# Optimization experiments

Measured on AMD Instinct MI355X. Metric: run time of the kernel, lower is better.

Reference implementation:

```python
import jax, jax.numpy as jnp
import numpy as np

NEG = -9.0e15

def gat_layer(X, adj_mask, W, Wb, a1, a2, ab):
    # X: [N, Fin]; W: [Fin, Fout]; a1,a2: [Fout]; ab: scalar
    h = X @ W + Wb                                   # [N, Fout]
    # a([h_i || h_j]) = h_i@a1 + h_j@a2 + ab  (decomposition of concat+linear)
    e = jax.nn.leaky_relu((h @ a1)[:, None] + (h @ a2)[None, :] + ab,
                          negative_slope=0.2)        # [N, N]
    e = jnp.where(adj_mask, e, NEG)
    attn = jax.nn.softmax(e, axis=1)                 # [N, N]
    return jax.nn.elu(attn @ h)                      # [N, Fout]

def setup_inputs() -> dict:
    key = jax.random.key(0)
    ks = jax.random.split(key, 12)
    N, Fin, Fh, H, Fout = 4096, 512, 128, 4, 64
    X = jax.random.normal(ks[0], (N, Fin), dtype=jnp.float32)
    adjacency_matrix = jax.random.randint(ks[1], (N, N), 0, 2, dtype=jnp.int32)
    s_in = 1.0 / np.sqrt(Fin)
    s_a = 1.0 / np.sqrt(2 * Fh)
    W_h  = jax.random.uniform(ks[2], (H, Fin, Fh), jnp.float32, -s_in, s_in)
    b_h  = jax.random.uniform(ks[3], (H, Fh), jnp.float32, -s_in, s_in)
    a1_h = jax.random.uniform(ks[4], (H, Fh), jnp.float32, -s_a, s_a)
    a2_h = jax.random.uniform(ks[5], (H, Fh), jnp.float32, -s_a, s_a)
    ab_h = jax.random.uniform(ks[6], (H,), jnp.float32, -s_a, s_a)
    Fcat = H * Fh
    s_c = 1.0 / np.sqrt(Fcat)
    s_ao = 1.0 / np.sqrt(2 * Fout)
    W_o  = jax.random.uniform(ks[7], (Fcat, Fout), jnp.float32, -s_c, s_c)
    b_o  = jax.random.uniform(ks[8], (Fout,), jnp.float32, -s_c, s_c)
    a1_o = jax.random.uniform(ks[9], (Fout,), jnp.float32, -s_ao, s_ao)
    a2_o = jax.random.uniform(ks[10], (Fout,), jnp.float32, -s_ao, s_ao)
    ab_o = jax.random.uniform(ks[11], (), jnp.float32, -s_ao, s_ao)
    return {"X": X, "adjacency_matrix": adjacency_matrix,
            "W_h": W_h, "b_h": b_h, "a1_h": a1_h, "a2_h": a2_h, "ab_h": ab_h,
            "W_o": W_o, "b_o": b_o, "a1_o": a1_o, "a2_o": a2_o, "ab_o": ab_o}

def reference(X, adjacency_matrix, W_h, b_h, a1_h, a2_h, ab_h,
              W_o, b_o, a1_o, a2_o, ab_o):
    adj_mask = adjacency_matrix > 0
    # per-head attention layers, vmapped over heads
    heads = jax.vmap(gat_layer, in_axes=(None, None, 0, 0, 0, 0, 0))(
        X, adj_mask, W_h, b_h, a1_h, a2_h, ab_h)      # [H, N, Fh]
    H, N, Fh = heads.shape
    x = jnp.transpose(heads, (1, 0, 2)).reshape(N, H * Fh)  # concat along features
    x = gat_layer(x, adj_mask, W_o, b_o, a1_o, a2_o, ab_o)  # [N, Fout]
    return jax.nn.log_softmax(x, axis=1)
```

## Files before the change

### kernel.cpp

```cpp
#include <hip/hip_runtime.h>
#include <math.h>

#define NN 4096

using f32x4  = __attribute__((ext_vector_type(4))) float;
using bf16x4 = __attribute__((ext_vector_type(4))) __bf16;
using bf16x8 = __attribute__((ext_vector_type(8))) __bf16;

__device__ __forceinline__ void barrier_lgkm() {
    asm volatile("s_waitcnt lgkmcnt(0)\ns_barrier" ::: "memory");
}

template<int FH>
__device__ __forceinline__ void stage_tile(const __bf16* __restrict__ hgp,
                                           __bf16* dst, int tid) {
#pragma unroll
    for (int it = 0; it < FH / 32; it++) {
        int c = tid + it * 256;
        int f = c >> 3, sl = c & 7;
        int g = sl ^ (f & 7);
        __builtin_amdgcn_global_load_lds(
            (const __attribute__((address_space(1))) void*)(hgp + (size_t)f * NN + g * 8),
            (__attribute__((address_space(3))) void*)(dst + (size_t)c * 8), 16, 0, 0);
    }
}

__device__ __forceinline__ void stage_g(const __bf16* __restrict__ base, int ldk,
                                        __bf16* dst, int tid) {
#pragma unroll
    for (int it = 0; it < 2; it++) {
        int c = tid + it * 256;
        int f = c >> 3, sl = c & 7;
        int g = sl ^ (f & 7);
        __builtin_amdgcn_global_load_lds(
            (const __attribute__((address_space(1))) void*)(base + (size_t)f * ldk + g * 8),
            (__attribute__((address_space(3))) void*)(dst + (size_t)c * 8), 16, 0, 0);
    }
}

__global__ void pack_adj_kernel(const int* __restrict__ adj,
                                unsigned long long* __restrict__ bits) {
    int gw = (blockIdx.x * blockDim.x + threadIdx.x) >> 6;
    int lane = threadIdx.x & 63;
    int v = adj[(size_t)gw * 64 + lane];
    unsigned long long m = __ballot(v > 0);
    if (lane == 0) bits[gw] = m;
}

__global__ void prepack_kernel(const float* __restrict__ W_h, const float* __restrict__ b_h,
                               const float* __restrict__ W_o,
                               __bf16* __restrict__ Bt1, float* __restrict__ biasp,
                               __bf16* __restrict__ Bt2) {
    int idx = blockIdx.x * 256 + threadIdx.x;
    {
        int n = idx >> 9, k = idx & 511;
        int h = n >> 7, f = n & 127;
        Bt1[idx] = (__bf16)W_h[(size_t)h * 512 * 128 + k * 128 + f];
    }
    if (idx < 64 * 512) {
        int n = idx >> 9, k = idx & 511;
        Bt2[idx] = (__bf16)W_o[k * 64 + n];
    }
    if (idx < 512) biasp[idx] = b_h[idx];
}

__global__ void cast_bf16_kernel(const float* __restrict__ src, __bf16* __restrict__ dst) {
    int i = blockIdx.x * 256 + threadIdx.x;
    f32x4 v = *(const f32x4*)(src + (size_t)i * 4);
    bf16x4 o;
#pragma unroll
    for (int q = 0; q < 4; q++) o[q] = (__bf16)v[q];
    *(bf16x4*)(dst + (size_t)i * 4) = o;
}

__global__ __launch_bounds__(256) void gemm_fused_kernel(
    const __bf16* __restrict__ A, const __bf16* __restrict__ Bt,
    const float* __restrict__ bias,
    const float* __restrict__ a1, const float* __restrict__ a2,
    __bf16* __restrict__ Ht, float* __restrict__ s1, float* __restrict__ s2,
    int M, int N, int K)
{
    __shared__ __attribute__((aligned(16))) __bf16 As[2][64 * 64];
    __shared__ __attribute__((aligned(16))) __bf16 Bs[2][64 * 64];
    const int tid = threadIdx.x, w = tid >> 6, l = tid & 63, o = l >> 4, rl = l & 15;
    const int bm = blockIdx.y * 64, bn = blockIdx.x * 64;
    f32x4 acc[4] = {};
    stage_g(A + (size_t)bm * K, K, &As[0][0], tid);
    stage_g(Bt + (size_t)bn * K, K, &Bs[0][0], tid);
    const int KB = K / 64;
    for (int kb = 0; kb < KB; kb++) {
        int b = kb & 1;
        __syncthreads();
        if (kb + 1 < KB) {
            stage_g(A + (size_t)bm * K + (kb + 1) * 64, K, &As[b ^ 1][0], tid);
            stage_g(Bt + (size_t)bn * K + (kb + 1) * 64, K, &Bs[b ^ 1][0], tid);
        }
#pragma unroll
        for (int kt = 0; kt < 2; kt++) {
            int ra = w * 16 + rl;
            int cg = kt * 4 + o;
            bf16x8 af = *(const bf16x8*)(&As[b][(ra * 8 + (cg ^ (ra & 7))) * 8]);
#pragma unroll
            for (int nt = 0; nt < 4; nt++) {
                int rb = nt * 16 + rl;
                bf16x8 bfr = *(const bf16x8*)(&Bs[b][(rb * 8 + (cg ^ (rb & 7))) * 8]);
                acc[nt] = __builtin_amdgcn_mfma_f32_16x16x32_bf16(af, bfr, acc[nt], 0, 0, 0);
            }
        }
    }
    const int head = bn >> 7;
    const int row_base = bm + w * 16 + o * 4;
    float p1[4] = {0.f, 0.f, 0.f, 0.f}, p2[4] = {0.f, 0.f, 0.f, 0.f};
#pragma unroll
    for (int nt = 0; nt < 4; nt++) {
        int col = bn + nt * 16 + rl;
        float bv = bias[col];
        float a1v = a1[col], a2v = a2[col];
        bf16x4 hv;
#pragma unroll
        for (int r4 = 0; r4 < 4; r4++) {
            float h = acc[nt][r4] + bv;
            hv[r4] = (__bf16)h;
            p1[r4] += h * a1v;
            p2[r4] += h * a2v;
        }
        *(bf16x4*)(Ht + (size_t)col * M + row_base) = hv;
    }
#pragma unroll
    for (int r4 = 0; r4 < 4; r4++)
#pragma unroll
        for (int off = 1; off < 16; off <<= 1) {
            p1[r4] += __shfl_xor(p1[r4], off, 64);
            p2[r4] += __shfl_xor(p2[r4], off, 64);
        }
    if (rl == 0)
#pragma unroll
        for (int r4 = 0; r4 < 4; r4++) {
            atomicAdd(&s1[(size_t)head * M + row_base + r4], p1[r4]);
            atomicAdd(&s2[(size_t)head * M + row_base + r4], p2[r4]);
        }
}

__global__ void smax_kernel(const float* __restrict__ s2, float* __restrict__ s2max) {
    const float* p = s2 + (size_t)blockIdx.x * NN;
    int t = threadIdx.x;
    float m = -INFINITY;
    for (int i = t; i < NN; i += 256) m = fmaxf(m, p[i]);
#pragma unroll
    for (int off = 1; off < 64; off <<= 1) m = fmaxf(m, __shfl_xor(m, off, 64));
    __shared__ float red[4];
    if ((t & 63) == 0) red[t >> 6] = m;
    __syncthreads();
    if (t == 0) s2max[blockIdx.x] = fmaxf(fmaxf(red[0], red[1]), fmaxf(red[2], red[3]));
}

template<int FH, int JSPLIT>
__global__ __launch_bounds__(256, 4) void attn_kernel(
    const __bf16* __restrict__ Htg,
    const unsigned long long* __restrict__ adj_bits,
    const float* __restrict__ s1_all, const float* __restrict__ s2_all,
    const float* __restrict__ s2max_all, const float* __restrict__ ab_all,
    __bf16* __restrict__ accp,
    float* __restrict__ lg,
    int ldo)
{
    constexpr int NJT = NN / 64 / JSPLIT;
    constexpr int NTW = FH / 64;
    const int head = blockIdx.y;
    const int js   = blockIdx.z;
    const int row0 = blockIdx.x * 64;
    const int jt0  = js * NJT;
    const int tid = threadIdx.x;
    const int w = tid >> 6, l = tid & 63, o = l >> 4, rl = l & 15;
    const int myrow = row0 + w * 16 + rl;

    __shared__ __attribute__((aligned(16))) __bf16 hbuf[2][FH * 64];
    __shared__ __attribute__((aligned(16))) __bf16 plds[8 * 64 * 8];

    const float* s2 = s2_all + (size_t)head * NN;
    const __bf16* hg = Htg + (size_t)head * FH * NN;
    const float s1r = s1_all[(size_t)head * NN + myrow] + ab_all[head];
    float mrow; { float x = s1r + s2max_all[head]; mrow = fmaxf(x, 0.2f * x); }
    float lacc = 0.f;
    f32x4 acc[4][NTW] = {};

    stage_tile<FH>(hg + (size_t)jt0 * 64, &hbuf[0][0], tid);

    for (int jl = 0; jl < NJT; jl++) {
        const int b = jl & 1;
        const int jt = jt0 + jl;
        unsigned long long aw = adj_bits[(size_t)myrow * 64 + jt];
        bf16x8 freg[2];
#pragma unroll
        for (int kt = 0; kt < 2; kt++) {
            unsigned int mbyte = (unsigned int)(aw >> ((kt * 4 + o) * 8)) & 0xFFu;
            int jb = jt * 64 + kt * 32 + o * 8;
            f32x4 sa = *(const f32x4*)(s2 + jb);
            f32x4 sb = *(const f32x4*)(s2 + jb + 4);
            float ps = 0.f;
#pragma unroll
            for (int q = 0; q < 8; q++) {
                float s2q = (q < 4) ? sa[q] : sb[q - 4];
                float x = s1r + s2q;
                float e = fmaxf(x, 0.2f * x);
                float p = ((mbyte >> q) & 1u) ? __expf(e - mrow) : 0.f;
                freg[kt][q] = (__bf16)p;
                ps += p;
            }
            ps += __shfl_xor(ps, 16, 64);
            ps += __shfl_xor(ps, 32, 64);
            lacc += ps;
            *(bf16x8*)(&plds[((w * 2 + kt) * 64 + l) * 8]) = freg[kt];
        }
        __syncthreads();
        if (jl + 1 < NJT)
            stage_tile<FH>(hg + (size_t)(jt + 1) * 64, &hbuf[b ^ 1][0], tid);
        bf16x8 bfr[2][NTW];
#pragma unroll
        for (int kt = 0; kt < 2; kt++)
#pragma unroll
            for (int ntl = 0; ntl < NTW; ntl++) {
                int f = (w * NTW + ntl) * 16 + rl;
                int slot = (kt * 4 + o) ^ (rl & 7);
                bfr[kt][ntl] = *(const bf16x8*)(&hbuf[b][(f * 8 + slot) * 8]);
            }
#pragma unroll
        for (int mt = 0; mt < 4; mt++)
#pragma unroll
            for (int kt = 0; kt < 2; kt++) {
                bf16x8 af = (mt == w) ? freg[kt]
                          : *(const bf16x8*)(&plds[((mt * 2 + kt) * 64 + l) * 8]);
#pragma unroll
                for (int ntl = 0; ntl < NTW; ntl++)
                    acc[mt][ntl] = __builtin_amdgcn_mfma_f32_16x16x32_bf16(
                        af, bfr[kt][ntl], acc[mt][ntl], 0, 0, 0);
            }
        barrier_lgkm();
    }
    if (l < 16) lg[((size_t)head * JSPLIT + js) * NN + row0 + w * 16 + l] = lacc;
#pragma unroll
    for (int mt = 0; mt < 4; mt++)
#pragma unroll
        for (int ntl = 0; ntl < NTW; ntl++)
#pragma unroll
            for (int r4 = 0; r4 < 4; r4++) {
                int grow = row0 + mt * 16 + o * 4 + r4;
                int gcol = head * FH + (w * NTW + ntl) * 16 + rl;
                accp[((size_t)js * NN + grow) * ldo + gcol] = (__bf16)acc[mt][ntl][r4];
            }
}

__global__ void combine1_kernel(const __bf16* __restrict__ accp, const float* __restrict__ lg,
                                __bf16* __restrict__ outb) {
    int gid = blockIdx.x * 256 + threadIdx.x;
    int row = gid >> 7, c4 = (gid & 127) * 4;
    int head = c4 >> 7;
    float lsum = 0.f;
#pragma unroll
    for (int js = 0; js < 4; js++) lsum += lg[((size_t)head * 4 + js) * NN + row];
    float inv = lsum > 0.f ? 1.f / lsum : 0.f;
    float v[4] = {0.f, 0.f, 0.f, 0.f};
#pragma unroll
    for (int js = 0; js < 4; js++) {
        bf16x4 t = *(const bf16x4*)(accp + ((size_t)js * NN + row) * 512 + c4);
#pragma unroll
        for (int q = 0; q < 4; q++) v[q] += (float)t[q];
    }
    bf16x4 ob;
#pragma unroll
    for (int q = 0; q < 4; q++) {
        float x = v[q] * inv;
        x = x > 0.f ? x : __expf(x) - 1.f;
        ob[q] = (__bf16)x;
    }
    *(bf16x4*)(outb + (size_t)row * 512 + c4) = ob;
}

__global__ void combine2_kernel(const __bf16* __restrict__ accp, const float* __restrict__ lg,
                                float* __restrict__ out) {
    int row = (blockIdx.x * 256 + threadIdx.x) >> 6;
    int lane = threadIdx.x & 63;
    if (row >= NN) return;
    float lsum = 0.f, v = 0.f;
#pragma unroll
    for (int js = 0; js < 16; js++) {
        lsum += lg[(size_t)js * NN + row];
        v += (float)accp[((size_t)js * NN + row) * 64 + lane];
    }
    float inv = lsum > 0.f ? 1.f / lsum : 0.f;
    v *= inv;
    v = v > 0.f ? v : __expf(v) - 1.f;
    float m = v;
#pragma unroll
    for (int off = 1; off < 64; off <<= 1) m = fmaxf(m, __shfl_xor(m, off, 64));
    float ex = __expf(v - m);
    float s = ex;
#pragma unroll
    for (int off = 1; off < 64; off <<= 1) s += __shfl_xor(s, off, 64);
    out[(size_t)row * 64 + lane] = v - m - __logf(s);
}

extern "C" void kernel_launch(void* const* d_in, const int* in_sizes, int n_in,
                              void* d_out, int out_size, void* d_ws, size_t ws_size,
                              hipStream_t stream) {
    const float* X    = (const float*)d_in[0];
    const int*   adj  = (const int*)d_in[1];
    const float* W_h  = (const float*)d_in[2];
    const float* b_h  = (const float*)d_in[3];
    const float* a1_h = (const float*)d_in[4];
    const float* a2_h = (const float*)d_in[5];
    const float* ab_h = (const float*)d_in[6];
    const float* W_o  = (const float*)d_in[7];
    const float* b_o  = (const float*)d_in[8];
    const float* a1_o = (const float*)d_in[9];
    const float* a2_o = (const float*)d_in[10];
    const float* ab_o = (const float*)d_in[11];
    float* out = (float*)d_out;

    char* ws = (char*)d_ws;
    auto alloc = [&](size_t bytes) {
        char* p = ws; ws += (bytes + 255) & ~(size_t)255; return p;
    };
    unsigned long long* adj_bits = (unsigned long long*)alloc((size_t)NN * 64 * 8);
    __bf16* Bt1    = (__bf16*)alloc((size_t)512 * 512 * 2);
    float*  biasp  = (float*)alloc(512 * 4);
    __bf16* Bt2    = (__bf16*)alloc((size_t)64 * 512 * 2);
    __bf16* Xb     = (__bf16*)alloc((size_t)NN * 512 * 2);
    float*  s1h    = (float*)alloc((size_t)4 * NN * 4);
    float*  s2h    = (float*)alloc((size_t)4 * NN * 4);
    float*  s1o    = (float*)alloc((size_t)NN * 4);
    float*  s2o    = (float*)alloc((size_t)NN * 4);
    float*  s2maxh = (float*)alloc(4 * 4);
    float*  s2maxo = (float*)alloc(4);
    __bf16* Htg    = (__bf16*)alloc((size_t)512 * NN * 2);
    __bf16* accp1  = (__bf16*)alloc((size_t)4 * NN * 512 * 2);
    float*  lg1    = (float*)alloc((size_t)16 * NN * 4);
    __bf16* outhb  = (__bf16*)alloc((size_t)NN * 512 * 2);
    __bf16* Ht2    = (__bf16*)alloc((size_t)64 * NN * 2);
    __bf16* accp2  = (__bf16*)alloc((size_t)16 * NN * 64 * 2);
    float*  lg2    = (float*)alloc((size_t)16 * NN * 4);

    hipMemsetAsync(s1h, 0, (size_t)(4 + 4 + 1 + 1) * NN * 4, stream);
    pack_adj_kernel<<<(NN * 64) / 4, 256, 0, stream>>>(adj, adj_bits);
    prepack_kernel<<<1024, 256, 0, stream>>>(W_h, b_h, W_o, Bt1, biasp, Bt2);
    cast_bf16_kernel<<<(NN * 512 / 4) / 256, 256, 0, stream>>>(X, Xb);
    gemm_fused_kernel<<<dim3(8, 64), 256, 0, stream>>>(
        Xb, Bt1, biasp, a1_h, a2_h, Htg, s1h, s2h, NN, 512, 512);
    smax_kernel<<<4, 256, 0, stream>>>(s2h, s2maxh);
    attn_kernel<128, 4><<<dim3(NN / 64, 4, 4), 256, 0, stream>>>(
        Htg, adj_bits, s1h, s2h, s2maxh, ab_h, accp1, lg1, 512);
    combine1_kernel<<<(NN * 128) / 256, 256, 0, stream>>>(accp1, lg1, outhb);
    gemm_fused_kernel<<<dim3(1, 64), 256, 0, stream>>>(
        outhb, Bt2, b_o, a1_o, a2_o, Ht2, s1o, s2o, NN, 64, 512);
    smax_kernel<<<1, 256, 0, stream>>>(s2o, s2maxo);
    attn_kernel<64, 16><<<dim3(NN / 64, 1, 16), 256, 0, stream>>>(
        Ht2, adj_bits, s1o, s2o, s2maxo, ab_o, accp2, lg2, 64);
    combine2_kernel<<<(NN * 64) / 256, 256, 0, stream>>>(accp2, lg2, out);
}
```

Measured before the change: 232.3 us.

## Factor attention exponentials into precomputed per-column terms and restructure attn tiling

The per-element exp in the attention kernel becomes a product of a per-row factor and a precomputed per-column exponential. It picks one of two branches depending on the sign of the leaky-relu input, and a new prep kernel builds the column factors alongside the max. Each wave now owns 32 rows and all feature columns, which removes the shared P staging buffer and the trailing barrier. The first layer's j-split grows from 4 to 8, and the second layer uses 128-thread blocks. The cost is twice the partial-accumulator traffic in combine1, plus possible precision loss in the factored exponentials.

```diff
diff --git a/kernel.cpp b/kernel.cpp
--- a/kernel.cpp
+++ b/kernel.cpp
@@ -7,16 +7,12 @@
 using bf16x4 = __attribute__((ext_vector_type(4))) __bf16;
 using bf16x8 = __attribute__((ext_vector_type(8))) __bf16;
 
-__device__ __forceinline__ void barrier_lgkm() {
-    asm volatile("s_waitcnt lgkmcnt(0)\ns_barrier" ::: "memory");
-}
-
-template<int FH>
+template<int FH, int NTH>
 __device__ __forceinline__ void stage_tile(const __bf16* __restrict__ hgp,
                                            __bf16* dst, int tid) {
 #pragma unroll
-    for (int it = 0; it < FH / 32; it++) {
-        int c = tid + it * 256;
+    for (int it = 0; it < FH * 8 / NTH; it++) {
+        int c = tid + it * NTH;
         int f = c >> 3, sl = c & 7;
         int g = sl ^ (f & 7);
         __builtin_amdgcn_global_load_lds(
@@ -141,112 +137,136 @@
         }
 }
 
-__global__ void smax_kernel(const float* __restrict__ s2, float* __restrict__ s2max) {
-    const float* p = s2 + (size_t)blockIdx.x * NN;
-    int t = threadIdx.x;
+__global__ void attn_prep_kernel(const float* __restrict__ s2_all,
+                                 float* __restrict__ s2max_all,
+                                 float* __restrict__ BD) {
+    const int head = blockIdx.x;
+    const float* s2 = s2_all + (size_t)head * NN;
+    const int t = threadIdx.x;
     float m = -INFINITY;
-    for (int i = t; i < NN; i += 256) m = fmaxf(m, p[i]);
+    for (int i = t; i < NN; i += 256) m = fmaxf(m, s2[i]);
 #pragma unroll
     for (int off = 1; off < 64; off <<= 1) m = fmaxf(m, __shfl_xor(m, off, 64));
     __shared__ float red[4];
     if ((t & 63) == 0) red[t >> 6] = m;
     __syncthreads();
-    if (t == 0) s2max[blockIdx.x] = fmaxf(fmaxf(red[0], red[1]), fmaxf(red[2], red[3]));
-}
-
-template<int FH, int JSPLIT>
-__global__ __launch_bounds__(256, 4) void attn_kernel(
+    float smax = fmaxf(fmaxf(red[0], red[1]), fmaxf(red[2], red[3]));
+    if (t == 0) s2max_all[head] = smax;
+    float* Bv = BD + (size_t)head * 2 * NN;
+    float* Dv = Bv + NN;
+    for (int i = t; i < NN; i += 256) {
+        float d = s2[i] - smax;
+        Bv[i] = __expf(d);
+        Dv[i] = __expf(0.2f * d);
+    }
+}
+
+template<int FH, int JSPLIT, int WAVES>
+__global__ __launch_bounds__(WAVES * 64, 4) void attn_kernel(
     const __bf16* __restrict__ Htg,
     const unsigned long long* __restrict__ adj_bits,
-    const float* __restrict__ s1_all, const float* __restrict__ s2_all,
+    const float* __restrict__ s1_all, const float* __restrict__ BD,
     const float* __restrict__ s2max_all, const float* __restrict__ ab_all,
     __bf16* __restrict__ accp,
     float* __restrict__ lg,
     int ldo)
 {
     constexpr int NJT = NN / 64 / JSPLIT;
-    constexpr int NTW = FH / 64;
-    const int head = blockIdx.y;
-    const int js   = blockIdx.z;
-    const int row0 = blockIdx.x * 64;
+    constexpr int NT  = FH / 16;
+    const int head = blockIdx.y, js = blockIdx.z;
+    const int row0 = blockIdx.x * (WAVES * 32);
     const int jt0  = js * NJT;
     const int tid = threadIdx.x;
     const int w = tid >> 6, l = tid & 63, o = l >> 4, rl = l & 15;
-    const int myrow = row0 + w * 16 + rl;
+    const int rbase = row0 + w * 32;
 
     __shared__ __attribute__((aligned(16))) __bf16 hbuf[2][FH * 64];
-    __shared__ __attribute__((aligned(16))) __bf16 plds[8 * 64 * 8];
-
-    const float* s2 = s2_all + (size_t)head * NN;
+
+    const float* Bv = BD + (size_t)head * 2 * NN;
+    const float* Dv = Bv + NN;
     const __bf16* hg = Htg + (size_t)head * FH * NN;
-    const float s1r = s1_all[(size_t)head * NN + myrow] + ab_all[head];
-    float mrow; { float x = s1r + s2max_all[head]; mrow = fmaxf(x, 0.2f * x); }
-    float lacc = 0.f;
-    f32x4 acc[4][NTW] = {};
-
-    stage_tile<FH>(hg + (size_t)jt0 * 64, &hbuf[0][0], tid);
-
+    const float smax = s2max_all[head];
+    const float abh = ab_all[head];
+
+    float Au[2], Cu[2], Tb[2], lacc[2] = {0.f, 0.f};
+    const unsigned long long* awp[2];
+#pragma unroll
+    for (int mt = 0; mt < 2; mt++) {
+        int row = rbase + mt * 16 + rl;
+        float z = s1_all[(size_t)head * NN + row] + abh + smax;
+        float mr = fmaxf(z, 0.2f * z);
+        Au[mt] = __expf(z - mr);
+        Cu[mt] = __expf(0.2f * z - mr);
+        Tb[mt] = __expf(fminf(-z, 80.f));
+        awp[mt] = adj_bits + (size_t)row * 64;
+    }
+    f32x4 acc[2][NT] = {};
+
+    stage_tile<FH, WAVES * 64>(hg + (size_t)jt0 * 64, &hbuf[0][0], tid);
+
+#pragma unroll 2
     for (int jl = 0; jl < NJT; jl++) {
         const int b = jl & 1;
         const int jt = jt0 + jl;
-        unsigned long long aw = adj_bits[(size_t)myrow * 64 + jt];
-        bf16x8 freg[2];
+        unsigned long long aw0 = awp[0][jt], aw1 = awp[1][jt];
+        bf16x8 af[2][2];
 #pragma unroll
         for (int kt = 0; kt < 2; kt++) {
-            unsigned int mbyte = (unsigned int)(aw >> ((kt * 4 + o) * 8)) & 0xFFu;
             int jb = jt * 64 + kt * 32 + o * 8;
-            f32x4 sa = *(const f32x4*)(s2 + jb);
-            f32x4 sb = *(const f32x4*)(s2 + jb + 4);
-            float ps = 0.f;
+            f32x4 b0 = *(const f32x4*)(Bv + jb);
+            f32x4 b1 = *(const f32x4*)(Bv + jb + 4);
+            f32x4 d0 = *(const f32x4*)(Dv + jb);
+            f32x4 d1 = *(const f32x4*)(Dv + jb + 4);
+            unsigned int mb0 = (unsigned int)(aw0 >> ((kt * 4 + o) * 8)) & 0xFFu;
+            unsigned int mb1 = (unsigned int)(aw1 >> ((kt * 4 + o) * 8)) & 0xFFu;
 #pragma unroll
             for (int q = 0; q < 8; q++) {
-                float s2q = (q < 4) ? sa[q] : sb[q - 4];
-                float x = s1r + s2q;
-                float e = fmaxf(x, 0.2f * x);
-                float p = ((mbyte >> q) & 1u) ? __expf(e - mrow) : 0.f;
-                freg[kt][q] = (__bf16)p;
-                ps += p;
+                float bq = (q < 4) ? b0[q] : b1[q - 4];
+                float dq = (q < 4) ? d0[q] : d1[q - 4];
+                float p0 = (bq >= Tb[0]) ? Au[0] * bq : Cu[0] * dq;
+                p0 = ((mb0 >> q) & 1u) ? p0 : 0.f;
+                af[0][kt][q] = (__bf16)p0;
+                lacc[0] += p0;
+                float p1 = (bq >= Tb[1]) ? Au[1] * bq : Cu[1] * dq;
+                p1 = ((mb1 >> q) & 1u) ? p1 : 0.f;
+                af[1][kt][q] = (__bf16)p1;
+                lacc[1] += p1;
             }
-            ps += __shfl_xor(ps, 16, 64);
-            ps += __shfl_xor(ps, 32, 64);
-            lacc += ps;
-            *(bf16x8*)(&plds[((w * 2 + kt) * 64 + l) * 8]) = freg[kt];
         }
         __syncthreads();
         if (jl + 1 < NJT)
-            stage_tile<FH>(hg + (size_t)(jt + 1) * 64, &hbuf[b ^ 1][0], tid);
-        bf16x8 bfr[2][NTW];
-#pragma unroll
-        for (int kt = 0; kt < 2; kt++)
-#pragma unroll
-            for (int ntl = 0; ntl < NTW; ntl++) {
-                int f = (w * NTW + ntl) * 16 + rl;
+            stage_tile<FH, WAVES * 64>(hg + (size_t)(jt + 1) * 64, &hbuf[b ^ 1][0], tid);
+#pragma unroll
+        for (int kt = 0; kt < 2; kt++) {
+#pragma unroll
+            for (int nt = 0; nt < NT; nt++) {
+                int f = nt * 16 + rl;
                 int slot = (kt * 4 + o) ^ (rl & 7);
-                bfr[kt][ntl] = *(const bf16x8*)(&hbuf[b][(f * 8 + slot) * 8]);
+                bf16x8 bfr = *(const bf16x8*)(&hbuf[b][(f * 8 + slot) * 8]);
+                acc[0][nt] = __builtin_amdgcn_mfma_f32_16x16x32_bf16(af[0][kt], bfr, acc[0][nt], 0, 0, 0);
+                acc[1][nt] = __builtin_amdgcn_mfma_f32_16x16x32_bf16(af[1][kt], bfr, acc[1][nt], 0, 0, 0);
             }
-#pragma unroll
-        for (int mt = 0; mt < 4; mt++)
-#pragma unroll
-            for (int kt = 0; kt < 2; kt++) {
-                bf16x8 af = (mt == w) ? freg[kt]
-                          : *(const bf16x8*)(&plds[((mt * 2 + kt) * 64 + l) * 8]);
-#pragma unroll
-                for (int ntl = 0; ntl < NTW; ntl++)
-                    acc[mt][ntl] = __builtin_amdgcn_mfma_f32_16x16x32_bf16(
-                        af, bfr[kt][ntl], acc[mt][ntl], 0, 0, 0);
-            }
-        barrier_lgkm();
-    }
-    if (l < 16) lg[((size_t)head * JSPLIT + js) * NN + row0 + w * 16 + l] = lacc;
-#pragma unroll
-    for (int mt = 0; mt < 4; mt++)
-#pragma unroll
-        for (int ntl = 0; ntl < NTW; ntl++)
+        }
+    }
+#pragma unroll
+    for (int mt = 0; mt < 2; mt++) {
+        lacc[mt] += __shfl_xor(lacc[mt], 16, 64);
+        lacc[mt] += __shfl_xor(lacc[mt], 32, 64);
+    }
+    if (l < 16) {
+        float* lgp = lg + ((size_t)head * JSPLIT + js) * NN + rbase;
+        lgp[l] = lacc[0];
+        lgp[16 + l] = lacc[1];
+    }
+#pragma unroll
+    for (int mt = 0; mt < 2; mt++)
+#pragma unroll
+        for (int nt = 0; nt < NT; nt++)
 #pragma unroll
             for (int r4 = 0; r4 < 4; r4++) {
-                int grow = row0 + mt * 16 + o * 4 + r4;
-                int gcol = head * FH + (w * NTW + ntl) * 16 + rl;
-                accp[((size_t)js * NN + grow) * ldo + gcol] = (__bf16)acc[mt][ntl][r4];
+                int grow = rbase + mt * 16 + o * 4 + r4;
+                int gcol = head * FH + nt * 16 + rl;
+                accp[((size_t)js * NN + grow) * ldo + gcol] = (__bf16)acc[mt][nt][r4];
             }
 }
 
@@ -257,11 +277,11 @@
     int head = c4 >> 7;
     float lsum = 0.f;
 #pragma unroll
-    for (int js = 0; js < 4; js++) lsum += lg[((size_t)head * 4 + js) * NN + row];
+    for (int js = 0; js < 8; js++) lsum += lg[((size_t)head * 8 + js) * NN + row];
     float inv = lsum > 0.f ? 1.f / lsum : 0.f;
     float v[4] = {0.f, 0.f, 0.f, 0.f};
 #pragma unroll
-    for (int js = 0; js < 4; js++) {
+    for (int js = 0; js < 8; js++) {
         bf16x4 t = *(const bf16x4*)(accp + ((size_t)js * NN + row) * 512 + c4);
 #pragma unroll
         for (int q = 0; q < 4; q++) v[q] += (float)t[q];
@@ -332,9 +352,11 @@
     float*  s2o    = (float*)alloc((size_t)NN * 4);
     float*  s2maxh = (float*)alloc(4 * 4);
     float*  s2maxo = (float*)alloc(4);
+    float*  BDh    = (float*)alloc((size_t)4 * 2 * NN * 4);
+    float*  BDo    = (float*)alloc((size_t)2 * NN * 4);
     __bf16* Htg    = (__bf16*)alloc((size_t)512 * NN * 2);
-    __bf16* accp1  = (__bf16*)alloc((size_t)4 * NN * 512 * 2);
-    float*  lg1    = (float*)alloc((size_t)16 * NN * 4);
+    __bf16* accp1  = (__bf16*)alloc((size_t)8 * NN * 512 * 2);
+    float*  lg1    = (float*)alloc((size_t)32 * NN * 4);
     __bf16* outhb  = (__bf16*)alloc((size_t)NN * 512 * 2);
     __bf16* Ht2    = (__bf16*)alloc((size_t)64 * NN * 2);
     __bf16* accp2  = (__bf16*)alloc((size_t)16 * NN * 64 * 2);
@@ -346,14 +368,14 @@
     cast_bf16_kernel<<<(NN * 512 / 4) / 256, 256, 0, stream>>>(X, Xb);
     gemm_fused_kernel<<<dim3(8, 64), 256, 0, stream>>>(
         Xb, Bt1, biasp, a1_h, a2_h, Htg, s1h, s2h, NN, 512, 512);
-    smax_kernel<<<4, 256, 0, stream>>>(s2h, s2maxh);
-    attn_kernel<128, 4><<<dim3(NN / 64, 4, 4), 256, 0, stream>>>(
-        Htg, adj_bits, s1h, s2h, s2maxh, ab_h, accp1, lg1, 512);
+    attn_prep_kernel<<<4, 256, 0, stream>>>(s2h, s2maxh, BDh);
+    attn_kernel<128, 8, 4><<<dim3(NN / 128, 4, 8), 256, 0, stream>>>(
+        Htg, adj_bits, s1h, BDh, s2maxh, ab_h, accp1, lg1, 512);
     combine1_kernel<<<(NN * 128) / 256, 256, 0, stream>>>(accp1, lg1, outhb);
     gemm_fused_kernel<<<dim3(1, 64), 256, 0, stream>>>(
         outhb, Bt2, b_o, a1_o, a2_o, Ht2, s1o, s2o, NN, 64, 512);
-    smax_kernel<<<1, 256, 0, stream>>>(s2o, s2maxo);
-    attn_kernel<64, 16><<<dim3(NN / 64, 1, 16), 256, 0, stream>>>(
-        Ht2, adj_bits, s1o, s2o, s2maxo, ab_o, accp2, lg2, 64);
+    attn_prep_kernel<<<1, 256, 0, stream>>>(s2o, s2maxo, BDo);
+    attn_kernel<64, 16, 2><<<dim3(NN / 64, 1, 16), 128, 0, stream>>>(
+        Ht2, adj_bits, s1o, BDo, s2maxo, ab_o, accp2, lg2, 64);
     combine2_kernel<<<(NN * 64) / 256, 256, 0, stream>>>(accp2, lg2, out);
 }
```

New measurement: 338.6 us. 1.46x slower.
